# Kernel tuning notes

Measured on AMD Instinct MI355X. Metric: run time of the kernel, lower is better.

Reference implementation:

```python
import jax, jax.numpy as jnp
import numpy as np

BN_EPS = 1e-5
STRIDE = 12          # ACCENT_DOWNSAMPLE_STRIDE
NQ = 8               # ACCENT_VQ_QUANTIZERS
K = 256              # ACCENT_VQ_CODEBOOK_SIZE
VQ_D = 16            # ACCENT_VQ_DIM
EMB = 128            # ACCENT_EMBEDDING_DIM


def conv1d(x, w, b, stride=1, padding=0):
    # x: (B, Cin, T), w: (Cout, Cin, Kw)
    y = jax.lax.conv_general_dilated(
        x, w, window_strides=(stride,), padding=[(padding, padding)],
        dimension_numbers=("NCW", "OIW", "NCW"))
    return y + b[None, :, None]


def batchnorm(x, gamma, beta, mean, var):
    # eval-mode BatchNorm1d over channel dim
    inv = jax.lax.rsqrt(var + BN_EPS)
    return (x - mean[None, :, None]) * (inv * gamma)[None, :, None] + beta[None, :, None]


def setup_inputs() -> dict:
    key = jax.random.key(0)
    ks = jax.random.split(key, 12)
    C = 256
    d = {
        "mel_spectrogram": jax.random.normal(ks[0], (16, 80, 4096), jnp.float32),
        "w1": jax.random.normal(ks[1], (C, 80, 5), jnp.float32) * 0.05,
        "b1": jnp.zeros((C,), jnp.float32),
        "g1": jnp.ones((C,), jnp.float32),
        "be1": jnp.zeros((C,), jnp.float32),
        "m1": jax.random.normal(ks[2], (C,), jnp.float32) * 0.1,
        "v1": jax.random.uniform(ks[3], (C,), jnp.float32, 0.5, 1.5),
        "w2": jax.random.normal(ks[4], (C, C, 5), jnp.float32) * 0.03,
        "b2": jnp.zeros((C,), jnp.float32),
        "g2": jnp.ones((C,), jnp.float32),
        "be2": jnp.zeros((C,), jnp.float32),
        "m2": jax.random.normal(ks[5], (C,), jnp.float32) * 0.1,
        "v2": jax.random.uniform(ks[6], (C,), jnp.float32, 0.5, 1.5),
        "wd": jax.random.normal(ks[7], (EMB, C, 2 * STRIDE), jnp.float32) * 0.02,
        "bd": jnp.zeros((EMB,), jnp.float32),
        "wp": jax.random.normal(ks[8], (VQ_D, EMB, 1), jnp.float32) * 0.1,
        "bp": jnp.zeros((VQ_D,), jnp.float32),
        "codebooks": jax.random.normal(ks[9], (NQ, K, VQ_D), jnp.float32) * 0.3,
    }
    return d


def reference(mel_spectrogram, w1, b1, g1, be1, m1, v1,
              w2, b2, g2, be2, m2, v2, wd, bd, wp, bp, codebooks):
    # CNN stack
    x = jax.nn.relu(batchnorm(conv1d(mel_spectrogram, w1, b1, 1, 2), g1, be1, m1, v1))
    x = jax.nn.relu(batchnorm(conv1d(x, w2, b2, 1, 2), g2, be2, m2, v2))
    # Downsample conv: kernel=24, stride=12, pad=6
    e_a_unq = conv1d(x, wd, bd, STRIDE, STRIDE // 2)          # (B, 128, T')
    z = conv1d(e_a_unq, wp, bp, 1, 0)                          # (B, 16, T')
    # RVQ: 8 sequential cdist-argmin-subtract steps
    r = jnp.transpose(z, (0, 2, 1))                            # (B, T', 16)
    idx_list = []
    for q in range(NQ):
        cb = codebooks[q]                                      # (K, 16)
        # squared euclidean distances (B, T', K)
        d = (jnp.sum(r * r, -1, keepdims=True)
             - 2.0 * jnp.einsum("btd,kd->btk", r, cb)
             + jnp.sum(cb * cb, -1))
        idx = jnp.argmin(d, axis=-1)                           # (B, T')
        idx_list.append(idx)
        r = r - cb[idx]                                        # residual update
    indices = jnp.stack(idx_list, axis=0)                      # (NQ, B, T')
    return e_a_unq, indices
```

## Files before the change

kernel.cpp:

```cpp
#include <hip/hip_runtime.h>
#include <math.h>

#define B_    16
#define BCH   4
#define T_    4096
#define C_    256
#define CIN1  80
#define EMB   128
#define TP    341
#define NPOS  (B_*TP)
#define NQ_   8
#define KCB   256
#define BN_EPS 1e-5

__global__ __launch_bounds__(256) void prep_f64(
    const float* __restrict__ w1, const float* __restrict__ w2,
    const float* __restrict__ wd,
    const float* __restrict__ b1, const float* __restrict__ g1,
    const float* __restrict__ be1, const float* __restrict__ m1,
    const float* __restrict__ v1,
    const float* __restrict__ b2, const float* __restrict__ g2,
    const float* __restrict__ be2, const float* __restrict__ m2,
    const float* __restrict__ v2,
    const float* __restrict__ wp, const float* __restrict__ bp,
    double* __restrict__ w1t, double* __restrict__ w2t, double* __restrict__ wdt,
    double* __restrict__ a1, double* __restrict__ bt1,
    double* __restrict__ a2, double* __restrict__ bt2,
    double* __restrict__ wpd, double* __restrict__ bpd)
{
    int j = blockIdx.x * 256 + threadIdx.x;
    if (j < 256*24*128) wdt[j] = (double)wd[(size_t)(j & 127) * 6144 + (j >> 7)];
    if (j < 256*5*256)  w2t[j] = (double)w2[(size_t)(j & 255) * 1280 + (j >> 8)];
    if (j < 80*5*256)   w1t[j] = (double)w1[(size_t)(j & 255) * 400 + (j >> 8)];
    if (j < 16*128)     wpd[j] = (double)wp[j];
    if (j < 16)         bpd[j] = (double)bp[j];
    if (j < 256) {
        double inv1 = 1.0 / sqrt((double)v1[j] + BN_EPS);
        double s1 = (double)g1[j] * inv1;
        a1[j]  = s1;
        bt1[j] = ((double)b1[j] - (double)m1[j]) * s1 + (double)be1[j];
        double inv2 = 1.0 / sqrt((double)v2[j] + BN_EPS);
        double s2 = (double)g2[j] * inv2;
        a2[j]  = s2;
        bt2[j] = ((double)b2[j] - (double)m2[j]) * s2 + (double)be2[j];
    }
}

template<int CIN, typename Tin>
__global__ __launch_bounds__(256) void conv5_bn_relu_f64(
    const Tin* __restrict__ in,
    const double* __restrict__ wt,
    const double* __restrict__ alpha, const double* __restrict__ beta,
    double* __restrict__ out)
{
    const int b   = blockIdx.z;
    const int co0 = blockIdx.y * 64;
    const int t0  = blockIdx.x * 128;
    const int tid = threadIdx.x;
    const int tcol = tid & 15;
    const int trow = tid >> 4;

    __shared__ double xs[16][136];
    __shared__ double wsh[80][64];

    double acc[4][8];
    #pragma unroll
    for (int i = 0; i < 4; ++i)
        #pragma unroll
        for (int j = 0; j < 8; ++j) acc[i][j] = 0.0;

    for (int c0 = 0; c0 < CIN; c0 += 16) {
        for (int i = tid; i < 16 * 132; i += 256) {
            int ci = i / 132, col = i % 132;
            int t = t0 - 2 + col;
            double v = 0.0;
            if (t >= 0 && t < T_) v = (double)in[((size_t)(b * CIN + c0 + ci)) * T_ + t];
            xs[ci][col] = v;
        }
        for (int i = tid; i < 80 * 64; i += 256) {
            int r = i >> 6, co = i & 63;
            wsh[r][co] = wt[(size_t)(c0 * 5 + r) * 256 + co0 + co];
        }
        __syncthreads();

        for (int ci = 0; ci < 16; ++ci) {
            double xv[12];
            #pragma unroll
            for (int j = 0; j < 12; ++j) xv[j] = xs[ci][tcol * 8 + j];
            #pragma unroll
            for (int k = 0; k < 5; ++k) {
                double w0 = wsh[ci * 5 + k][trow * 4 + 0];
                double w1v = wsh[ci * 5 + k][trow * 4 + 1];
                double w2v = wsh[ci * 5 + k][trow * 4 + 2];
                double w3v = wsh[ci * 5 + k][trow * 4 + 3];
                #pragma unroll
                for (int j = 0; j < 8; ++j) {
                    double xq = xv[j + k];
                    acc[0][j] = fma(w0, xq, acc[0][j]);
                    acc[1][j] = fma(w1v, xq, acc[1][j]);
                    acc[2][j] = fma(w2v, xq, acc[2][j]);
                    acc[3][j] = fma(w3v, xq, acc[3][j]);
                }
            }
        }
        __syncthreads();
    }

    const int cobase = co0 + trow * 4;
    const int tg = t0 + tcol * 8;
    #pragma unroll
    for (int i = 0; i < 4; ++i) {
        double a = alpha[cobase + i], bt = beta[cobase + i];
        size_t base = ((size_t)(b * C_ + cobase + i)) * T_ + tg;
        #pragma unroll
        for (int j = 0; j < 8; ++j) {
            double y = fma(acc[i][j], a, bt);
            out[base + j] = y > 0.0 ? y : 0.0;
        }
    }
}

__global__ __launch_bounds__(256) void convd_f64_v4(
    const double* __restrict__ x2,
    const double* __restrict__ wdt,
    double* __restrict__ parts,
    int nb)
{
    const int bz  = blockIdx.z;
    const int s   = bz & 3;
    const int b   = bz >> 2;
    const int co0 = blockIdx.y * 64;
    const int tp0 = blockIdx.x * 64;
    const int tid = threadIdx.x;
    const int tcol = tid & 15;
    const int crow = tid >> 4;
    const int ci0 = s * 64;

    __shared__ double xs[2][780];
    __shared__ double wsh[48][64];

    double acc[4][4];
    #pragma unroll
    for (int i = 0; i < 4; ++i)
        #pragma unroll
        for (int j = 0; j < 4; ++j) acc[i][j] = 0.0;

    const int tbase = tp0 * 12 - 6;

    for (int c0 = ci0; c0 < ci0 + 64; c0 += 2) {
        for (int i = tid; i < 2 * 780; i += 256) {
            int ci = i / 780, col = i % 780;
            int t = tbase + col;
            xs[ci][col] = (t >= 0 && t < T_)
                ? x2[((size_t)(b * 256 + c0 + ci)) * T_ + t] : 0.0;
        }
        for (int i = tid; i < 48 * 64; i += 256) {
            int r = i >> 6, c = i & 63;
            wsh[r][c] = wdt[(size_t)(c0 * 24 + r) * 128 + co0 + c];
        }
        __syncthreads();

        #pragma unroll
        for (int ci = 0; ci < 2; ++ci) {
            #pragma unroll
            for (int k = 0; k < 24; k += 2) {
                double2 wa0 = *(const double2*)&wsh[ci * 24 + k][crow * 4];
                double2 wa1 = *(const double2*)&wsh[ci * 24 + k][crow * 4 + 2];
                double2 wb0 = *(const double2*)&wsh[ci * 24 + k + 1][crow * 4];
                double2 wb1 = *(const double2*)&wsh[ci * 24 + k + 1][crow * 4 + 2];
                #pragma unroll
                for (int j = 0; j < 4; ++j) {
                    double2 xp = *(const double2*)&xs[ci][(tcol * 4 + j) * 12 + k];
                    acc[0][j] = fma(wa0.x, xp.x, acc[0][j]);
                    acc[1][j] = fma(wa0.y, xp.x, acc[1][j]);
                    acc[2][j] = fma(wa1.x, xp.x, acc[2][j]);
                    acc[3][j] = fma(wa1.y, xp.x, acc[3][j]);
                    acc[0][j] = fma(wb0.x, xp.y, acc[0][j]);
                    acc[1][j] = fma(wb0.y, xp.y, acc[1][j]);
                    acc[2][j] = fma(wb1.x, xp.y, acc[2][j]);
                    acc[3][j] = fma(wb1.y, xp.y, acc[3][j]);
                }
            }
        }
        __syncthreads();
    }

    #pragma unroll
    for (int i = 0; i < 4; ++i) {
        int co = co0 + crow * 4 + i;
        #pragma unroll
        for (int j = 0; j < 4; ++j) {
            int tp = tp0 + tcol * 4 + j;
            if (tp < TP)
                parts[(((size_t)s * nb + b) * EMB + co) * TP + tp] = acc[i][j];
        }
    }
}

__global__ __launch_bounds__(256) void convd_combine(
    const double* __restrict__ parts,
    const float* __restrict__ bd,
    double* __restrict__ ed,
    float* __restrict__ e_out,
    int nb, int b_off)
{
    int idx = blockIdx.x * 256 + threadIdx.x;
    int total = nb * EMB * TP;
    if (idx >= total) return;
    int b_local = idx / (EMB * TP);
    int rem = idx % (EMB * TP);
    int co = rem / TP;
    size_t stride = (size_t)nb * EMB * TP;
    double y = parts[idx];
    y += parts[stride + idx];
    y += parts[2 * stride + idx];
    y += parts[3 * stride + idx];
    y += (double)bd[co];
    size_t o = (size_t)(b_off + b_local) * EMB * TP + rem;
    ed[o] = y;
    e_out[o] = (float)y;
}

__global__ __launch_bounds__(128) void zproj_f64(
    const double* __restrict__ ed,
    const double* __restrict__ wpd,
    const double* __restrict__ bpd,
    double* __restrict__ z)
{
    const int b = blockIdx.y;
    const int t = blockIdx.x * 128 + threadIdx.x;
    __shared__ double wps[16][128];
    for (int i = threadIdx.x; i < 16 * 128; i += 128)
        wps[i >> 7][i & 127] = wpd[i];
    __syncthreads();
    if (t >= TP) return;
    double acc[16];
    #pragma unroll
    for (int v = 0; v < 16; ++v) acc[v] = bpd[v];
    for (int co = 0; co < 128; ++co) {
        double x = ed[((size_t)(b * EMB + co)) * TP + t];
        #pragma unroll
        for (int v = 0; v < 16; ++v) acc[v] = fma(x, wps[v][co], acc[v]);
    }
    #pragma unroll
    for (int v = 0; v < 16; ++v)
        z[((size_t)(b * TP + t)) * 16 + v] = acc[v];
}

__global__ __launch_bounds__(256) void rvq_f64_v2(
    const double* __restrict__ z,
    const float* __restrict__ cb,
    float* __restrict__ out_idx)
{
    const int pos = blockIdx.x;
    const int tid = threadIdx.x;
    const int lane = tid & 63;
    const int wv = tid >> 6;

    __shared__ double r[16];
    __shared__ double wd_s[4];
    __shared__ int wi_s[4];
    __shared__ int best_s;

    if (tid < 16) r[tid] = z[(size_t)pos * 16 + tid];
    __syncthreads();

    for (int q = 0; q < NQ_; ++q) {
        const float* c = cb + ((size_t)(q * KCB) + tid) * 16;
        double d = 0.0;
        #pragma unroll
        for (int i = 0; i < 16; ++i) {
            double diff = r[i] - (double)c[i];
            d = fma(diff, diff, d);
        }
        int idx = tid;
        #pragma unroll
        for (int sft = 32; sft > 0; sft >>= 1) {
            double d2 = __shfl_down(d, sft, 64);
            int i2 = __shfl_down(idx, sft, 64);
            if (d2 < d || (d2 == d && i2 < idx)) { d = d2; idx = i2; }
        }
        if (lane == 0) { wd_s[wv] = d; wi_s[wv] = idx; }
        __syncthreads();
        if (tid == 0) {
            double bd_ = wd_s[0]; int bi = wi_s[0];
            #pragma unroll
            for (int w = 1; w < 4; ++w) {
                if (wd_s[w] < bd_ || (wd_s[w] == bd_ && wi_s[w] < bi)) {
                    bd_ = wd_s[w]; bi = wi_s[w];
                }
            }
            best_s = bi;
            out_idx[(size_t)q * NPOS + pos] = (float)bi;
        }
        __syncthreads();
        int best = best_s;
        if (tid < 16)
            r[tid] = r[tid] - (double)cb[((size_t)(q * KCB) + best) * 16 + tid];
        __syncthreads();
    }
}

extern "C" void kernel_launch(void* const* d_in, const int* in_sizes, int n_in,
                              void* d_out, int out_size, void* d_ws, size_t ws_size,
                              hipStream_t stream) {
    const float* mel = (const float*)d_in[0];
    const float* w1  = (const float*)d_in[1];
    const float* b1  = (const float*)d_in[2];
    const float* g1  = (const float*)d_in[3];
    const float* be1 = (const float*)d_in[4];
    const float* m1  = (const float*)d_in[5];
    const float* v1  = (const float*)d_in[6];
    const float* w2  = (const float*)d_in[7];
    const float* b2  = (const float*)d_in[8];
    const float* g2  = (const float*)d_in[9];
    const float* be2 = (const float*)d_in[10];
    const float* m2  = (const float*)d_in[11];
    const float* v2  = (const float*)d_in[12];
    const float* wd  = (const float*)d_in[13];
    const float* bd  = (const float*)d_in[14];
    const float* wp  = (const float*)d_in[15];
    const float* bp  = (const float*)d_in[16];
    const float* cb  = (const float*)d_in[17];

    auto need = [](int nb) -> size_t {
        size_t s = 0;
        s += (size_t)BCH * C_ * T_ * 8;
        s += (size_t)nb * C_ * T_ * 8;
        s += (size_t)80*5*256*8 + (size_t)256*5*256*8 + (size_t)256*24*128*8;
        s += 6 * 4096;
        s += (size_t)16 * EMB * TP * 8;
        s += (size_t)16 * TP * 16 * 8;
        s += (size_t)4 * nb * EMB * TP * 8;
        s += 64 * 1024;
        return s;
    };
    const int nb = (ws_size >= need(16)) ? 16 : 8;
    const int ngrp = B_ / nb;

    char* ws = (char*)d_ws;
    size_t off = 0;
    auto alloc = [&](size_t bytes) -> char* {
        char* p = ws + off;
        off = (off + bytes + 255) & ~(size_t)255;
        return p;
    };
    double* x1d  = (double*)alloc((size_t)BCH * C_ * T_ * 8);
    double* x2d  = (double*)alloc((size_t)nb * C_ * T_ * 8);
    double* w1td = (double*)alloc((size_t)80*5*256*8);
    double* w2td = (double*)alloc((size_t)256*5*256*8);
    double* wdtd = (double*)alloc((size_t)256*24*128*8);
    double* a1d  = (double*)alloc(2048);
    double* bt1d = (double*)alloc(2048);
    double* a2d  = (double*)alloc(2048);
    double* bt2d = (double*)alloc(2048);
    double* wpd  = (double*)alloc(16*128*8);
    double* bpd  = (double*)alloc(16*8);
    double* ed   = (double*)alloc((size_t)16 * EMB * TP * 8);
    double* zd   = (double*)alloc((size_t)16 * TP * 16 * 8);
    double* parts= (double*)alloc((size_t)4 * nb * EMB * TP * 8);

    float* e_out   = (float*)d_out;
    float* idx_out = (float*)d_out + (size_t)B_ * EMB * TP;

    prep_f64<<<3072, 256, 0, stream>>>(w1, w2, wd, b1, g1, be1, m1, v1,
                                       b2, g2, be2, m2, v2, wp, bp,
                                       w1td, w2td, wdtd, a1d, bt1d, a2d, bt2d,
                                       wpd, bpd);

    const int comb_blocks = (nb * EMB * TP + 255) / 256;
    for (int g = 0; g < ngrp; ++g) {
        for (int ch = 0; ch < nb / BCH; ++ch) {
            int ch_abs = g * (nb / BCH) + ch;
            const float* mel_c = mel + (size_t)ch_abs * BCH * CIN1 * T_;
            conv5_bn_relu_f64<CIN1, float><<<dim3(32, 4, BCH), 256, 0, stream>>>(
                mel_c, w1td, a1d, bt1d, x1d);
            conv5_bn_relu_f64<C_, double><<<dim3(32, 4, BCH), 256, 0, stream>>>(
                x1d, w2td, a2d, bt2d, x2d + (size_t)ch * BCH * C_ * T_);
        }
        convd_f64_v4<<<dim3(6, 2, nb * 4), 256, 0, stream>>>(x2d, wdtd, parts, nb);
        convd_combine<<<comb_blocks, 256, 0, stream>>>(parts, bd, ed, e_out,
                                                       nb, g * nb);
    }
    zproj_f64<<<dim3(3, 16), 128, 0, stream>>>(ed, wpd, bpd, zd);
    rvq_f64_v2<<<NPOS, 256, 0, stream>>>(zd, cb, idx_out);
}
```

Before: 1.866 ms.

## Retile fp64 downsample conv, swizzle shared-memory input, halve conv5 channel chunk

The downsample conv now gives each thread an 8x4 output tile over 128 time positions, and the input-channel split into partial sums is a runtime parameter (8 splits when workspace allows), with the combine kernel looping over splits. Shared-memory input rows are stored with an XOR swizzle on double pairs to cut LDS bank conflicts, and conv5 stages 8 input channels per tile instead of 16, with vectorized double2 reads and an unrolled channel loop. The aim is more FMAs per shared-memory load, fewer bank conflicts, and higher occupancy from less shared memory. The trade-offs are higher register pressure, more partial-sum traffic and twice as many barriers in conv5.

```diff
diff --git a/kernel.cpp b/kernel.cpp
--- a/kernel.cpp
+++ b/kernel.cpp
@@ -46,6 +46,15 @@
     }
 }
 
+__device__ __forceinline__ int swz_pair(int col) {
+    int bw = col >> 1;
+    return ((bw ^ ((bw >> 3) & 7)) << 1);
+}
+__device__ __forceinline__ int swz_scalar(int col) {
+    int bw = col >> 1;
+    return (((bw ^ ((bw >> 3) & 7)) << 1) | (col & 1));
+}
+
 template<int CIN, typename Tin>
 __global__ __launch_bounds__(256) void conv5_bn_relu_f64(
     const Tin* __restrict__ in,
@@ -60,8 +69,8 @@
     const int tcol = tid & 15;
     const int trow = tid >> 4;
 
-    __shared__ double xs[16][136];
-    __shared__ double wsh[80][64];
+    __shared__ double xs[8][136];
+    __shared__ double wsh[40][64];
 
     double acc[4][8];
     #pragma unroll
@@ -69,24 +78,28 @@
         #pragma unroll
         for (int j = 0; j < 8; ++j) acc[i][j] = 0.0;
 
-    for (int c0 = 0; c0 < CIN; c0 += 16) {
-        for (int i = tid; i < 16 * 132; i += 256) {
+    for (int c0 = 0; c0 < CIN; c0 += 8) {
+        for (int i = tid; i < 8 * 132; i += 256) {
             int ci = i / 132, col = i % 132;
             int t = t0 - 2 + col;
             double v = 0.0;
             if (t >= 0 && t < T_) v = (double)in[((size_t)(b * CIN + c0 + ci)) * T_ + t];
-            xs[ci][col] = v;
-        }
-        for (int i = tid; i < 80 * 64; i += 256) {
+            xs[ci][swz_scalar(col)] = v;
+        }
+        for (int i = tid; i < 40 * 64; i += 256) {
             int r = i >> 6, co = i & 63;
             wsh[r][co] = wt[(size_t)(c0 * 5 + r) * 256 + co0 + co];
         }
         __syncthreads();
 
-        for (int ci = 0; ci < 16; ++ci) {
+        #pragma unroll
+        for (int ci = 0; ci < 8; ++ci) {
             double xv[12];
             #pragma unroll
-            for (int j = 0; j < 12; ++j) xv[j] = xs[ci][tcol * 8 + j];
+            for (int m = 0; m < 6; ++m) {
+                double2 v = *(const double2*)&xs[ci][swz_pair(tcol * 8 + 2 * m)];
+                xv[2 * m] = v.x; xv[2 * m + 1] = v.y;
+            }
             #pragma unroll
             for (int k = 0; k < 5; ++k) {
                 double w0 = wsh[ci * 5 + k][trow * 4 + 0];
@@ -120,39 +133,40 @@
     }
 }
 
-__global__ __launch_bounds__(256) void convd_f64_v4(
+__global__ __launch_bounds__(256) void convd_f64_v5(
     const double* __restrict__ x2,
     const double* __restrict__ wdt,
     double* __restrict__ parts,
-    int nb)
+    int nb, int nsplit, int cis)
 {
     const int bz  = blockIdx.z;
-    const int s   = bz & 3;
-    const int b   = bz >> 2;
+    const int s   = bz % nsplit;
+    const int b   = bz / nsplit;
     const int co0 = blockIdx.y * 64;
-    const int tp0 = blockIdx.x * 64;
+    const int tp0 = blockIdx.x * 128;
     const int tid = threadIdx.x;
-    const int tcol = tid & 15;
-    const int crow = tid >> 4;
-    const int ci0 = s * 64;
-
-    __shared__ double xs[2][780];
+    const int tcol = tid & 31;
+    const int crow = tid >> 5;
+
+    __shared__ double xs[2][1552];
     __shared__ double wsh[48][64];
 
-    double acc[4][4];
-    #pragma unroll
-    for (int i = 0; i < 4; ++i)
+    double acc[8][4];
+    #pragma unroll
+    for (int i = 0; i < 8; ++i)
         #pragma unroll
         for (int j = 0; j < 4; ++j) acc[i][j] = 0.0;
 
     const int tbase = tp0 * 12 - 6;
-
-    for (int c0 = ci0; c0 < ci0 + 64; c0 += 2) {
-        for (int i = tid; i < 2 * 780; i += 256) {
-            int ci = i / 780, col = i % 780;
+    const int ci_begin = s * cis;
+
+    for (int c0 = ci_begin; c0 < ci_begin + cis; c0 += 2) {
+        for (int i = tid; i < 2 * 1548; i += 256) {
+            int ci = i / 1548, col = i % 1548;
             int t = tbase + col;
-            xs[ci][col] = (t >= 0 && t < T_)
+            double v = (t >= 0 && t < T_)
                 ? x2[((size_t)(b * 256 + c0 + ci)) * T_ + t] : 0.0;
+            xs[ci][swz_scalar(col)] = v;
         }
         for (int i = tid; i < 48 * 64; i += 256) {
             int r = i >> 6, c = i & 63;
@@ -163,22 +177,24 @@
         #pragma unroll
         for (int ci = 0; ci < 2; ++ci) {
             #pragma unroll
-            for (int k = 0; k < 24; k += 2) {
-                double2 wa0 = *(const double2*)&wsh[ci * 24 + k][crow * 4];
-                double2 wa1 = *(const double2*)&wsh[ci * 24 + k][crow * 4 + 2];
-                double2 wb0 = *(const double2*)&wsh[ci * 24 + k + 1][crow * 4];
-                double2 wb1 = *(const double2*)&wsh[ci * 24 + k + 1][crow * 4 + 2];
+            for (int kk = 0; kk < 12; ++kk) {
+                const double* wr0 = &wsh[ci * 24 + 2 * kk][crow * 8];
+                const double* wr1 = &wsh[ci * 24 + 2 * kk + 1][crow * 8];
+                double2 xp[4];
                 #pragma unroll
                 for (int j = 0; j < 4; ++j) {
-                    double2 xp = *(const double2*)&xs[ci][(tcol * 4 + j) * 12 + k];
-                    acc[0][j] = fma(wa0.x, xp.x, acc[0][j]);
-                    acc[1][j] = fma(wa0.y, xp.x, acc[1][j]);
-                    acc[2][j] = fma(wa1.x, xp.x, acc[2][j]);
-                    acc[3][j] = fma(wa1.y, xp.x, acc[3][j]);
-                    acc[0][j] = fma(wb0.x, xp.y, acc[0][j]);
-                    acc[1][j] = fma(wb0.y, xp.y, acc[1][j]);
-                    acc[2][j] = fma(wb1.x, xp.y, acc[2][j]);
-                    acc[3][j] = fma(wb1.y, xp.y, acc[3][j]);
+                    int bw = (tcol + 32 * j) * 6 + kk;
+                    int colp = ((bw ^ ((bw >> 3) & 7)) << 1);
+                    xp[j] = *(const double2*)&xs[ci][colp];
+                }
+                #pragma unroll
+                for (int i = 0; i < 8; ++i) {
+                    double wa = wr0[i], wb = wr1[i];
+                    #pragma unroll
+                    for (int j = 0; j < 4; ++j) {
+                        acc[i][j] = fma(wa, xp[j].x, acc[i][j]);
+                        acc[i][j] = fma(wb, xp[j].y, acc[i][j]);
+                    }
                 }
             }
         }
@@ -186,11 +202,11 @@
     }
 
     #pragma unroll
-    for (int i = 0; i < 4; ++i) {
-        int co = co0 + crow * 4 + i;
+    for (int i = 0; i < 8; ++i) {
+        int co = co0 + crow * 8 + i;
         #pragma unroll
         for (int j = 0; j < 4; ++j) {
-            int tp = tp0 + tcol * 4 + j;
+            int tp = tp0 + tcol + 32 * j;
             if (tp < TP)
                 parts[(((size_t)s * nb + b) * EMB + co) * TP + tp] = acc[i][j];
         }
@@ -202,7 +218,7 @@
     const float* __restrict__ bd,
     double* __restrict__ ed,
     float* __restrict__ e_out,
-    int nb, int b_off)
+    int nb, int b_off, int nsplit)
 {
     int idx = blockIdx.x * 256 + threadIdx.x;
     int total = nb * EMB * TP;
@@ -211,10 +227,9 @@
     int rem = idx % (EMB * TP);
     int co = rem / TP;
     size_t stride = (size_t)nb * EMB * TP;
-    double y = parts[idx];
-    y += parts[stride + idx];
-    y += parts[2 * stride + idx];
-    y += parts[3 * stride + idx];
+    double y = 0.0;
+    for (int s = 0; s < nsplit; ++s)
+        y += parts[(size_t)s * stride + idx];
     y += (double)bd[co];
     size_t o = (size_t)(b_off + b_local) * EMB * TP + rem;
     ed[o] = y;
@@ -323,20 +338,23 @@
     const float* bp  = (const float*)d_in[16];
     const float* cb  = (const float*)d_in[17];
 
-    auto need = [](int nb) -> size_t {
+    auto need = [](int nb, int ns) -> size_t {
         size_t s = 0;
         s += (size_t)BCH * C_ * T_ * 8;
         s += (size_t)nb * C_ * T_ * 8;
         s += (size_t)80*5*256*8 + (size_t)256*5*256*8 + (size_t)256*24*128*8;
-        s += 6 * 4096;
+        s += 4 * 2048 + 16384 + 256;
         s += (size_t)16 * EMB * TP * 8;
         s += (size_t)16 * TP * 16 * 8;
-        s += (size_t)4 * nb * EMB * TP * 8;
-        s += 64 * 1024;
+        s += (size_t)ns * nb * EMB * TP * 8;
+        s += 16384;
         return s;
     };
-    const int nb = (ws_size >= need(16)) ? 16 : 8;
+    int nb = 8, nsplit = 8;
+    if (ws_size >= need(16, 8))      { nb = 16; nsplit = 8; }
+    else if (ws_size >= need(16, 4)) { nb = 16; nsplit = 4; }
     const int ngrp = B_ / nb;
+    const int cis  = 256 / nsplit;
 
     char* ws = (char*)d_ws;
     size_t off = 0;
@@ -358,7 +376,7 @@
     double* bpd  = (double*)alloc(16*8);
     double* ed   = (double*)alloc((size_t)16 * EMB * TP * 8);
     double* zd   = (double*)alloc((size_t)16 * TP * 16 * 8);
-    double* parts= (double*)alloc((size_t)4 * nb * EMB * TP * 8);
+    double* parts= (double*)alloc((size_t)nsplit * nb * EMB * TP * 8);
 
     float* e_out   = (float*)d_out;
     float* idx_out = (float*)d_out + (size_t)B_ * EMB * TP;
@@ -378,9 +396,10 @@
             conv5_bn_relu_f64<C_, double><<<dim3(32, 4, BCH), 256, 0, stream>>>(
                 x1d, w2td, a2d, bt2d, x2d + (size_t)ch * BCH * C_ * T_);
         }
-        convd_f64_v4<<<dim3(6, 2, nb * 4), 256, 0, stream>>>(x2d, wdtd, parts, nb);
+        convd_f64_v5<<<dim3(3, 2, nb * nsplit), 256, 0, stream>>>(
+            x2d, wdtd, parts, nb, nsplit, cis);
         convd_combine<<<comb_blocks, 256, 0, stream>>>(parts, bd, ed, e_out,
-                                                       nb, g * nb);
+                                                       nb, g * nb, nsplit);
     }
     zproj_f64<<<dim3(3, 16), 128, 0, stream>>>(ed, wpd, bpd, zd);
     rvq_f64_v2<<<NPOS, 256, 0, stream>>>(zd, cb, idx_out);
```

New measurement: 1.662 ms. 10.9% less time.
